# Performance work log

Measured on AMD Instinct MI355X. Metric: run time of the kernel, lower is better.

The kernel has to match this reference:

```python
import jax, jax.numpy as jnp
import numpy as np

V = 50257      # vocab size
H = 512        # hidden size
S = 128        # source length
BEAM = 5       # beam width (matches beam_width=5 default)
TMAX = 32      # MAX_LENGTH decode cap
SOS, EOS = 1, 2
NEG = -1e9


def setup_inputs() -> dict:
    key = jax.random.key(0)
    ks = jax.random.split(key, 12)
    p = lambda k, shape: jax.random.normal(k, shape, jnp.float32) * 0.02
    return {
        "input_tokens": jax.random.randint(ks[0], (S,), 0, V),
        "embedding": p(ks[1], (V, H)),
        "enc_Wih": p(ks[2], (3 * H, H)),
        "enc_Whh": p(ks[3], (3 * H, H)),
        "enc_bih": jnp.zeros((3 * H,), jnp.float32),
        "enc_bhh": jnp.zeros((3 * H,), jnp.float32),
        "dec_Wih": p(ks[4], (3 * H, H)),
        "dec_Whh": p(ks[5], (3 * H, H)),
        "dec_bih": jnp.zeros((3 * H,), jnp.float32),
        "dec_bhh": jnp.zeros((3 * H,), jnp.float32),
        "W_concat": p(ks[6], (2 * H, H)),
        "W_vocab": p(ks[7], (H, V)),
    }


def gru_cell(x, h, Wih, Whh, bih, bhh):
    # x, h: [..., H]
    gi = x @ Wih.T + bih
    gh = h @ Whh.T + bhh
    ir, iz, inn = jnp.split(gi, 3, -1)
    hr, hz, hn = jnp.split(gh, 3, -1)
    r = jax.nn.sigmoid(ir + hr)
    z = jax.nn.sigmoid(iz + hz)
    n = jnp.tanh(inn + r * hn)
    return (1.0 - z) * n + z * h


def reference(input_tokens, embedding, enc_Wih, enc_Whh, enc_bih, enc_bhh,
              dec_Wih, dec_Whh, dec_bih, dec_bhh, W_concat, W_vocab):
    # ---- encoder: 1-layer GRU over source tokens ----
    src_emb = embedding[input_tokens]                       # [S, H]

    def enc_step(h, x):
        h2 = gru_cell(x, h, enc_Wih, enc_Whh, enc_bih, enc_bhh)
        return h2, h2

    enc_h, enc_out = jax.lax.scan(enc_step, jnp.zeros((H,), src_emb.dtype), src_emb)
    # enc_out: [S, H], enc_h: [H]

    def decode_step(tokens, hidden):
        # tokens: [B] int, hidden: [B, H]
        x = embedding[tokens]                               # [B, H]
        h = gru_cell(x, hidden, dec_Wih, dec_Whh, dec_bih, dec_bhh)
        attn = jax.nn.softmax(h @ enc_out.T, axis=-1)       # [B, S] Luong dot attention
        ctx = attn @ enc_out                                # [B, H]
        o = jnp.tanh(jnp.concatenate([h, ctx], -1) @ W_concat)
        logp = jax.nn.log_softmax(o @ W_vocab, axis=-1)     # [B, V]
        return logp, h

    # ---- batched beam search (GPU-resident equivalent of the heapq loop) ----
    tokens0 = jnp.full((BEAM,), SOS, jnp.int32)
    hidden0 = jnp.tile(enc_h[None], (BEAM, 1))
    scores0 = jnp.full((BEAM,), NEG, jnp.float32).at[0].set(0.0)
    fin0 = jnp.zeros((BEAM,), bool)
    len0 = jnp.ones((BEAM,), jnp.int32)
    seqs0 = jnp.zeros((BEAM, TMAX), jnp.int32)
    fin_row = jnp.full((V,), NEG, jnp.float32).at[EOS].set(0.0)

    def beam_step(state, t):
        tokens, hidden, scores, finished, lengths, seqs = state
        logp, h2 = decode_step(tokens, hidden)              # [BEAM, V]
        step_lp = jnp.where(finished[:, None], fin_row[None, :], logp)
        cand = scores[:, None] + step_lp                    # [BEAM, V]
        top_scores, flat = jax.lax.top_k(cand.reshape(-1), BEAM)
        parent = flat // V
        tok = (flat % V).astype(jnp.int32)
        par_fin = finished[parent]
        new_fin = par_fin | (tok == EOS)
        new_len = lengths[parent] + jnp.where(par_fin, 0, 1)
        new_seqs = seqs[parent].at[:, t].set(jnp.where(par_fin, 0, tok))
        return (tok, h2[parent], top_scores, new_fin, new_len, new_seqs), None

    state, _ = jax.lax.scan(beam_step, (tokens0, hidden0, scores0, fin0, len0, seqs0),
                            jnp.arange(TMAX))
    _, _, scores, _, lengths, seqs = state
    # length-normalized ranking, matching node.logp / node.leng sort
    norm = scores / lengths.astype(scores.dtype)
    order = jnp.argsort(-norm)
    return seqs[order], norm[order]
```

## Files before the change

### kernel.cpp

```cpp
#include <hip/hip_runtime.h>
#include <cstdint>
#include <cstddef>

#define V_SZ 50257
#define H_SZ 512
#define S_SZ 128
#define NBEAM 5
#define TMAXX 32
#define TOK_SOS 1
#define TOK_EOS 2
#define NEGINF (-1e9f)

#define GW 128
#define NT 512
#define GENC 16
#define COLS_PER_WG 393

#define BI_LEAF(l)  ((l)*32)
#define BI_ROOT     256
#define BI_REL(l)   (512 + (l)*32)
#define BI_ECNT     1024
#define BI_EREL     1056

#define OF_GI    0
#define OF_ENC   196608
#define OF_EW    262144
#define OF_H2    327680
#define OF_AL    332800
#define OF_OTOP  333440
#define OF_PV    336000
#define OF_PM    339200
#define OF_PS    339840
#define OF_SC    340480
#define OI_BASE  340488

template <typename T>
__device__ __forceinline__ T aload(const T* p){
  return __hip_atomic_load((T*)p, __ATOMIC_RELAXED, __HIP_MEMORY_SCOPE_AGENT);
}
template <typename T>
__device__ __forceinline__ void astore(T* p, T v){
  __hip_atomic_store(p, v, __ATOMIC_RELAXED, __HIP_MEMORY_SCOPE_AGENT);
}

__device__ __forceinline__ float wredsum(float a){
#pragma unroll
  for (int m = 32; m; m >>= 1) a += __shfl_xor(a, m, 64);
  return a;
}

template <typename F>
__device__ __forceinline__ void dbar(int* bi, int wid, F&& tail){
  __shared__ int s_last;
  int mygen = 0;
  __syncthreads();
  if (threadIdx.x == 0){
    int leaf = wid >> 4;
    mygen = aload(bi + BI_REL(leaf));
    __builtin_amdgcn_s_waitcnt(0);
    int lo = __hip_atomic_fetch_add(bi + BI_LEAF(leaf), 1, __ATOMIC_RELAXED, __HIP_MEMORY_SCOPE_AGENT);
    int last = 0;
    if (lo == 15){
      astore(bi + BI_LEAF(leaf), 0);
      __builtin_amdgcn_s_waitcnt(0);
      int ro = __hip_atomic_fetch_add(bi + BI_ROOT, 1, __ATOMIC_RELAXED, __HIP_MEMORY_SCOPE_AGENT);
      if (ro == (GW/16) - 1){
        astore(bi + BI_ROOT, 0);
        last = 1;
      }
    }
    if (!last){
      while (aload(bi + BI_REL(leaf)) == mygen) __builtin_amdgcn_s_sleep(4);
    }
    s_last = last;
  }
  __syncthreads();
  if (s_last){
    tail();
    __syncthreads();
    if (threadIdx.x == 0){
      __builtin_amdgcn_s_waitcnt(0);
#pragma unroll
      for (int l = 0; l < GW/16; ++l) astore(bi + BI_REL(l), mygen + 1);
    }
  }
  __syncthreads();
}

__global__ __launch_bounds__(256)
void k_gi(const int* __restrict__ toks, const float* __restrict__ emb,
          const float* __restrict__ eWih, const float* __restrict__ ebih,
          float* __restrict__ ws)
{
  float* fb = ws + 2048;
  float* gi = fb + OF_GI;
  const int tid = threadIdx.x, wid = blockIdx.x, lane = tid & 63, wvi = tid >> 6;
  int Wg = wid*4 + wvi;
  for (int it = 0; it < 192; ++it){
    int idx = Wg*192 + it;
    int s = idx / 1536, j = idx - s*1536;
    const float* er = emb + (size_t)toks[s]*H_SZ;
    const float* wr = eWih + (size_t)j*H_SZ;
    float a = 0.f;
#pragma unroll
    for (int u = 0; u < 8; ++u) a += er[u*64+lane]*wr[u*64+lane];
    a = wredsum(a);
    if (lane == 0) gi[idx] = a + ebih[j];
  }
  if (wid == 0){
    float* sc = fb + OF_SC;
    int* ib = (int*)(fb + OI_BASE);
    if (tid < NBEAM){
      sc[tid] = (tid==0) ? 0.f : NEGINF;
      ib[3200+tid] = TOK_SOS; ib[3208+tid] = 0; ib[3216+tid] = 1; ib[3224+tid] = 0;
    }
    for (int q = tid; q < 2*NBEAM*TMAXX; q += 256) ib[3232+q] = 0;
  }
}

__global__ __launch_bounds__(NT, 1)
void k_enc(const float* __restrict__ eWhh, const float* __restrict__ ebhh,
           float* __restrict__ ws)
{
  int* bi = (int*)ws;
  float* fb = ws + 2048;
  float* gi = fb + OF_GI;
  float* enc = fb + OF_ENC;
  const int tid = threadIdx.x, wid = blockIdx.x, lane = tid & 63, wvi = tid >> 6;
  const int i0 = wid*32;
  __shared__ float smF[96];

  float wreg[12][8];
#pragma unroll
  for (int dd = 0; dd < 12; ++dd){
    int d = wvi*12 + dd, g = d >> 5, il = d & 31;
    const float* wr = eWhh + (size_t)(g*512 + i0 + il)*H_SZ;
#pragma unroll
    for (int u = 0; u < 8; ++u) wreg[dd][u] = wr[u*64+lane];
  }

  for (int s = 0; s < S_SZ; ++s){
    float hreg[8];
    if (s == 0){
#pragma unroll
      for (int u = 0; u < 8; ++u) hreg[u] = 0.f;
    } else {
      const float* hp = enc + (size_t)(s-1)*H_SZ;
#pragma unroll
      for (int u = 0; u < 8; ++u) hreg[u] = aload(hp + u*64 + lane);
    }
#pragma unroll
    for (int dd = 0; dd < 12; ++dd){
      float a = 0.f;
#pragma unroll
      for (int u = 0; u < 8; ++u) a += wreg[dd][u]*hreg[u];
      a = wredsum(a);
      if (lane == 0) smF[wvi*12 + dd] = a;
    }
    __syncthreads();
    if (tid < 32){
      int i = i0 + tid;
      float gr = smF[tid], gz = smF[32+tid], gn = smF[64+tid];
      float gir = gi[s*1536 + i], giz = gi[s*1536 + 512 + i], gin = gi[s*1536 + 1024 + i];
      float hprev = (s==0) ? 0.f : aload(enc + (s-1)*H_SZ + i);
      float r = 1.f/(1.f + expf(-(gir + gr + ebhh[i])));
      float z = 1.f/(1.f + expf(-(giz + gz + ebhh[512+i])));
      float n = tanhf(gin + r*(gn + ebhh[1024+i]));
      astore(enc + s*H_SZ + i, (1.f - z)*n + z*hprev);
    }
    __syncthreads();
    if (tid == 0){
      int g = aload(bi + BI_EREL);
      __builtin_amdgcn_s_waitcnt(0);
      int lo = __hip_atomic_fetch_add(bi + BI_ECNT, 1, __ATOMIC_RELAXED, __HIP_MEMORY_SCOPE_AGENT);
      if (lo == GENC - 1){
        astore(bi + BI_ECNT, 0);
        __builtin_amdgcn_s_waitcnt(0);
        astore(bi + BI_EREL, g + 1);
      } else {
        while (aload(bi + BI_EREL) == g) __builtin_amdgcn_s_sleep(2);
      }
    }
    __syncthreads();
  }
}

__global__ __launch_bounds__(NT)
void k_ew(const float* __restrict__ Wc, float* __restrict__ ws)
{
  float* fb = ws + 2048;
  float* enc = fb + OF_ENC;
  float* EW  = fb + OF_EW;
  const int tid = threadIdx.x, wid = blockIdx.x;
  int jc = wid & 15, sb = wid >> 4;
  int jl = tid & 31, sl = (tid >> 5) & 15;
  int s = sb*16 + sl, j = jc*32 + jl;
  const float* er = enc + (size_t)s*H_SZ;
  const float* wc = Wc + (size_t)512*H_SZ;
  float a = 0.f;
  for (int k = 0; k < 512; ++k) a += er[k]*wc[(size_t)k*H_SZ + j];
  EW[s*H_SZ + j] = a;
}

__global__ __launch_bounds__(NT, 1)
void k_dec(const float* __restrict__ emb,
           const float* __restrict__ dWih, const float* __restrict__ dWhh,
           const float* __restrict__ dbih, const float* __restrict__ dbhh,
           const float* __restrict__ Wc,  const float* __restrict__ Wv,
           float* __restrict__ out, float* __restrict__ ws)
{
  const int wid = blockIdx.x, tid = threadIdx.x;
  const int lane = tid & 63, wvi = tid >> 6;
  int* bi = (int*)ws;
  float* fb = ws + 2048;
  float* enc  = fb + OF_ENC;
  float* EW   = fb + OF_EW;
  float* h2   = fb + OF_H2;
  float* al   = fb + OF_AL;
  float* otop = fb + OF_OTOP;
  float* pv   = fb + OF_PV;
  float* pm   = fb + OF_PM;
  float* ps   = fb + OF_PS;
  float* sc   = fb + OF_SC;
  int* ib   = (int*)(fb + OI_BASE);
  int* pidx = ib;
  int* tokA = ib + 3200;
  int* finA = ib + 3208;
  int* lenA = ib + 3216;
  int* parA = ib + 3224;
  int* seqA = ib + 3232;

  __shared__ float smF[1024];
  __shared__ int   smI[256];
  __shared__ float s_buf[2560];
  __shared__ float s_pp[648];

  for (int t = 0; t < TMAXX; ++t){
    float* h2new = h2 + (t & 1)*2560;
    float* h2old = h2 + ((t & 1) ^ 1)*2560;

    if (tid < NBEAM){ smI[tid] = aload(tokA + tid); smI[8 + tid] = t ? aload(parA + tid) : 0; }
    __syncthreads();
    if (t == 0){
      for (int q = tid; q < 2560; q += NT) s_buf[q] = enc[127*H_SZ + (q & 511)];
    } else {
      for (int q = tid; q < 2560; q += NT){
        int b = q >> 9;
        s_buf[q] = aload(h2old + smI[8 + b]*H_SZ + (q & 511));
      }
    }
    __syncthreads();
    {
      int i0 = wid*4;
      int mat = wvi >> 2;
      float srg[5][8];
      if (mat == 0){
#pragma unroll
        for (int b = 0; b < NBEAM; ++b){
          const float* sp = emb + (size_t)smI[b]*H_SZ;
#pragma unroll
          for (int u = 0; u < 8; ++u) srg[b][u] = sp[u*64+lane];
        }
      } else {
#pragma unroll
        for (int b = 0; b < NBEAM; ++b)
#pragma unroll
          for (int u = 0; u < 8; ++u) srg[b][u] = s_buf[b*512 + u*64 + lane];
      }
      for (int rr = 0; rr < 3; ++rr){
        int R = wvi*3 + rr;
        int rem = R - mat*12;
        int g = rem >> 2, il = rem & 3;
        const float* wr = ((mat==0) ? dWih : dWhh) + (size_t)(g*512 + i0 + il)*H_SZ;
        float wreg[8];
#pragma unroll
        for (int u = 0; u < 8; ++u) wreg[u] = wr[u*64+lane];
#pragma unroll
        for (int b = 0; b < NBEAM; ++b){
          float a = 0.f;
#pragma unroll
          for (int u = 0; u < 8; ++u) a += wreg[u]*srg[b][u];
          a = wredsum(a);
          if (lane == 0) smF[R*5 + b] = a;
        }
      }
      __syncthreads();
      if (tid < 20){
        int b = tid >> 2, il = tid & 3;
        int i = i0 + il;
        float ir  = smF[(0*12 + 0*4 + il)*5 + b] + dbih[i];
        float iz  = smF[(0*12 + 1*4 + il)*5 + b] + dbih[512+i];
        float inn = smF[(0*12 + 2*4 + il)*5 + b] + dbih[1024+i];
        float hr  = smF[(1*12 + 0*4 + il)*5 + b] + dbhh[i];
        float hz  = smF[(1*12 + 1*4 + il)*5 + b] + dbhh[512+i];
        float hn  = smF[(1*12 + 2*4 + il)*5 + b] + dbhh[1024+i];
        float r = 1.f/(1.f + expf(-(ir + hr)));
        float z = 1.f/(1.f + expf(-(iz + hz)));
        float n = tanhf(inn + r*hn);
        float hp = s_buf[b*512 + i];
        astore(h2new + b*H_SZ + i, (1.f - z)*n + z*hp);
      }
    }
    dbar(bi, wid, [&](){});

    for (int q = tid; q < 2560; q += NT) s_buf[q] = aload(h2new + q);
    __syncthreads();
    if (wvi < NBEAM){
      const float* er = enc + (size_t)wid*H_SZ;
      float a = 0.f;
#pragma unroll
      for (int u = 0; u < 8; ++u) a += er[u*64+lane]*s_buf[wvi*512 + u*64 + lane];
      a = wredsum(a);
      if (lane == 0) astore(al + wvi*S_SZ + wid, a);
    }
    if (tid < 320){
      int q = tid % 20, ksl = tid / 20;
      int f = wid*20 + q;
      int b = f >> 9, j = f & 511;
      float a = 0.f;
#pragma unroll 8
      for (int u = 0; u < 32; ++u){
        int k = ksl*32 + u;
        a += s_buf[b*512 + k]*Wc[(size_t)k*H_SZ + j];
      }
      smF[q*16 + ksl] = a;
    }
    __syncthreads();
    if (tid < 20){
      float a = 0.f;
#pragma unroll
      for (int u = 0; u < 16; ++u) a += smF[tid*16 + u];
      astore(otop + wid*20 + tid, a);
    }
    dbar(bi, wid, [&](){});

    if (wvi < NBEAM){
      float a1 = aload(al + wvi*S_SZ + lane), a2 = aload(al + wvi*S_SZ + 64 + lane);
      float m = fmaxf(a1, a2);
#pragma unroll
      for (int mm = 32; mm; mm >>= 1) m = fmaxf(m, __shfl_xor(m, mm, 64));
      float e1 = expf(a1 - m), e2 = expf(a2 - m);
      s_pp[wvi*128 + lane] = e1; s_pp[wvi*128 + 64 + lane] = e2;
      float ssv = wredsum(e1 + e2);
      if (lane == 0) s_pp[640 + wvi] = ssv;
    }
    __syncthreads();
    {
      float acc[5] = {0.f,0.f,0.f,0.f,0.f};
      for (int s2 = 0; s2 < 128; ++s2){
        float e = EW[(size_t)s2*H_SZ + tid];
#pragma unroll
        for (int b = 0; b < NBEAM; ++b) acc[b] += e*s_pp[b*128 + s2];
      }
#pragma unroll
      for (int b = 0; b < NBEAM; ++b)
        s_buf[b*512 + tid] = tanhf(aload(otop + b*512 + tid) + acc[b]/s_pp[640 + b]);
    }
    __syncthreads();
    {
      int vbase = wid*COLS_PER_WG;
      int v = vbase + tid;
      bool act = (tid < COLS_PER_WG) && (v < V_SZ);
      int vc = act ? v : vbase;
      const float* wp = Wv + vc;
      float a0=0.f,a1=0.f,a2=0.f,a3=0.f,a4=0.f;
      for (int hb = 0; hb < H_SZ; hb += 16){
        float wr[16];
#pragma unroll
        for (int u = 0; u < 16; ++u) wr[u] = wp[(size_t)(hb+u)*V_SZ];
#pragma unroll
        for (int u = 0; u < 16; ++u){
          float w = wr[u];
          a0 += w*s_buf[hb+u];
          a1 += w*s_buf[512+hb+u];
          a2 += w*s_buf[1024+hb+u];
          a3 += w*s_buf[1536+hb+u];
          a4 += w*s_buf[2048+hb+u];
        }
      }
      if (!act){ a0=a1=a2=a3=a4=-3e38f; }
      int myv = act ? v : 0x7FFFFFFF;
      float accs[5] = {a0,a1,a2,a3,a4};
#pragma unroll
      for (int b = 0; b < NBEAM; ++b){
        float x = accs[b];
        float m = x;
#pragma unroll
        for (int mm = 32; mm; mm >>= 1) m = fmaxf(m, __shfl_xor(m, mm, 64));
        float e = expf(x - m);
        float ssum = wredsum(e);
        float bv = x; int bc = myv;
        float w5[5]; int i5[5];
#pragma unroll
        for (int r = 0; r < 5; ++r){
          float cv2 = bv; int ci2 = bc;
#pragma unroll
          for (int mm = 32; mm; mm >>= 1){
            float ov = __shfl_xor(cv2, mm, 64); int oi = __shfl_xor(ci2, mm, 64);
            bool take = (ov > cv2) || (ov == cv2 && oi < ci2);
            cv2 = take ? ov : cv2; ci2 = take ? oi : ci2;
          }
          w5[r] = cv2; i5[r] = ci2;
          if (bc == ci2) bv = -3e38f;
        }
        if (lane == 0){
#pragma unroll
          for (int r = 0; r < 5; ++r){ smF[(wvi*5+b)*5+r] = w5[r]; smI[(wvi*5+b)*5+r] = i5[r]; }
          smF[300 + wvi*5 + b] = m;
          smF[360 + wvi*5 + b] = ssum;
        }
      }
      __syncthreads();
      if (tid < NBEAM){
        float M = -3.4e38f, Sv = 0.f;
#pragma unroll
        for (int w8 = 0; w8 < 8; ++w8){
          float m2 = smF[300 + w8*5 + tid], s2 = smF[360 + w8*5 + tid];
          if (m2 > M){ Sv = Sv*expf(M - m2) + s2; M = m2; }
          else       { Sv = Sv + s2*expf(m2 - M); }
        }
        astore(pm + wid*5 + tid, M); astore(ps + wid*5 + tid, Sv);
      }
      if (wvi < NBEAM){
        int b = wvi;
        float cval; int cidx;
        if (lane < 40){ cval = smF[((lane/5)*5 + b)*5 + (lane%5)]; cidx = smI[((lane/5)*5 + b)*5 + (lane%5)]; }
        else { cval = -3e38f; cidx = 0x7FFFFFFF; }
        float bv = cval; int bc = cidx;
#pragma unroll
        for (int r = 0; r < 5; ++r){
          float cv2 = bv; int ci2 = bc;
#pragma unroll
          for (int mm = 32; mm; mm >>= 1){
            float ov = __shfl_xor(cv2, mm, 64); int oi = __shfl_xor(ci2, mm, 64);
            bool take = (ov > cv2) || (ov == cv2 && oi < ci2);
            cv2 = take ? ov : cv2; ci2 = take ? oi : ci2;
          }
          if (lane == 0){ astore(pv + (wid*5+b)*5+r, cv2); astore(pidx + (wid*5+b)*5+r, ci2); }
          if (bc == ci2) bv = -3e38f;
        }
      }
    }
    dbar(bi, wid, [&](){
      int b5 = wvi;
      if (b5 < NBEAM){
        float m1 = aload(pm + lane*5 + b5), s1 = aload(ps + lane*5 + b5);
        float m2 = aload(pm + (64+lane)*5 + b5), s2 = aload(ps + (64+lane)*5 + b5);
        float M, Sv;
        if (m1 >= m2){ M = m1; Sv = s1 + s2*expf(m2 - m1); }
        else         { M = m2; Sv = s2 + s1*expf(m1 - m2); }
#pragma unroll
        for (int mm = 32; mm; mm >>= 1){
          float om = __shfl_xor(M, mm, 64), os = __shfl_xor(Sv, mm, 64);
          if (om > M){ Sv = Sv*expf(M - om) + os; M = om; }
          else       { Sv = Sv + os*expf(om - M); }
        }
        if (lane == 0){ smF[8 + b5] = M; smF[80 + b5] = logf(Sv); }
        float lv[5]; int li[5];
#pragma unroll
        for (int r = 0; r < 5; ++r){ lv[r] = aload(pv + (lane*5 + b5)*5 + r); li[r] = aload(pidx + (lane*5 + b5)*5 + r); }
        for (int r = 0; r < 5; ++r){
          float nv = aload(pv + ((64+lane)*5 + b5)*5 + r); int ni = aload(pidx + ((64+lane)*5 + b5)*5 + r);
          bool ins = (nv > lv[4]) || (nv == lv[4] && ni < li[4]);
          if (!ins) break;
          lv[4] = nv; li[4] = ni;
#pragma unroll
          for (int p = 4; p > 0; --p){
            bool sw = (lv[p] > lv[p-1]) || (lv[p] == lv[p-1] && li[p] < li[p-1]);
            if (sw){ float tv = lv[p]; lv[p] = lv[p-1]; lv[p-1] = tv;
                     int ti = li[p]; li[p] = li[p-1]; li[p-1] = ti; }
          }
        }
        float cv = lv[0]; int ci = li[0];
#pragma unroll
        for (int r = 0; r < 5; ++r){
          float xv = cv; int xi = ci;
#pragma unroll
          for (int mm = 32; mm; mm >>= 1){
            float ov = __shfl_xor(xv, mm, 64); int oi = __shfl_xor(xi, mm, 64);
            bool take = (ov > xv) || (ov == xv && oi < xi);
            xv = take ? ov : xv; xi = take ? oi : xi;
          }
          if (lane == 0){ smF[16 + b5*5 + r] = xv; smI[16 + b5*5 + r] = xi; }
          if (ci == xi){
            lv[0]=lv[1]; li[0]=li[1]; lv[1]=lv[2]; li[1]=li[2];
            lv[2]=lv[3]; li[2]=li[3]; lv[3]=lv[4]; li[3]=li[4];
            lv[4] = -3e38f; li[4] = 0x7FFFFFFF;
            cv = lv[0]; ci = li[0];
          }
        }
      }
      __syncthreads();
      if (wvi == 0){
        float cval = -3e38f; int cflat = 0x7FFFFFFF;
        int b = lane/5, k = lane - b*5;
        if (lane < 25){
          if (aload(finA + b)){
            if (k == 0){ cval = aload(sc + b) + 0.0f; cflat = b*V_SZ + TOK_EOS; }
          } else {
            cval = ((smF[16 + b*5 + k] - smF[8 + b]) - smF[80 + b]) + aload(sc + b);
            cflat = b*V_SZ + smI[16 + b*5 + k];
          }
        }
        float bv = cval; int bc = cflat;
#pragma unroll
        for (int r = 0; r < 5; ++r){
          float xv = bv; int xi = bc;
#pragma unroll
          for (int mm = 32; mm; mm >>= 1){
            float ov = __shfl_xor(xv, mm, 64); int oi = __shfl_xor(xi, mm, 64);
            bool take = (ov > xv) || (ov == xv && oi < xi);
            xv = take ? ov : xv; xi = take ? oi : xi;
          }
          if (lane == 0){ smF[48 + r] = xv; smI[48 + r] = xi; }
          if (bc == xi) bv = -3e38f;
        }
        if (lane < NBEAM){
          int r = lane;
          float nscore = smF[48 + r]; int nfl = smI[48 + r];
          int par = nfl / V_SZ; int tok = nfl - par*V_SZ;
          int ofin = aload(finA + par); int olen = aload(lenA + par);
          int nf = (ofin || tok == TOK_EOS) ? 1 : 0;
          int nl = olen + (ofin ? 0 : 1);
          astore(sc + r, nscore); astore(tokA + r, tok); astore(finA + r, nf);
          astore(lenA + r, nl); astore(parA + r, par);
          smI[56 + r] = par; smI[64 + r] = tok; smI[72 + r] = ofin; smI[80 + r] = nl;
          smF[56 + r] = nscore;
        }
      }
      __syncthreads();
      int cur = t & 1, nxt = 1 - cur;
      if (tid < 160){
        int r = tid >> 5, u = tid & 31;
        int par = smI[56 + r];
        int val = aload(seqA + cur*160 + par*32 + u);
        if (u == t) val = smI[72 + r] ? 0 : smI[64 + r];
        astore(seqA + nxt*160 + r*32 + u, val);
      }
      if (t == TMAXX - 1){
        __syncthreads();
        if (tid == 0){
          float nn[5];
#pragma unroll
          for (int r = 0; r < 5; ++r) nn[r] = smF[56 + r] / (float)smI[80 + r];
          int used = 0;
#pragma unroll
          for (int r = 0; r < 5; ++r){
            int best = -1;
            for (int q2 = 0; q2 < 5; ++q2){
              if (used & (1 << q2)) continue;
              if (best < 0 || nn[q2] > nn[best]) best = q2;
            }
            used |= (1 << best);
            smI[88 + r] = best; smF[64 + r] = nn[best];
          }
        }
        __syncthreads();
        if (tid < 160){
          int r = tid >> 5, u = tid & 31;
          int src = smI[88 + r];
          out[tid] = (float)aload(seqA + nxt*160 + src*32 + u);
        }
        if (tid >= 160 && tid < 165) out[tid] = smF[64 + (tid - 160)];
      }
    });
  }
}

extern "C" void kernel_launch(void* const* d_in, const int* in_sizes, int n_in,
                              void* d_out, int out_size, void* d_ws, size_t ws_size,
                              hipStream_t stream)
{
  (void)in_sizes; (void)n_in; (void)out_size; (void)ws_size;
  hipMemsetAsync(d_ws, 0, 8192, stream);
  float* ws = (float*)d_ws;
  k_gi<<<dim3(256), dim3(256), 0, stream>>>(
      (const int*)d_in[0], (const float*)d_in[1],
      (const float*)d_in[2], (const float*)d_in[4], ws);
  k_enc<<<dim3(GENC), dim3(NT), 0, stream>>>(
      (const float*)d_in[3], (const float*)d_in[5], ws);
  k_ew<<<dim3(128), dim3(NT), 0, stream>>>(
      (const float*)d_in[10], ws);
  k_dec<<<dim3(GW), dim3(NT), 0, stream>>>(
      (const float*)d_in[1],
      (const float*)d_in[6], (const float*)d_in[7],
      (const float*)d_in[8], (const float*)d_in[9],
      (const float*)d_in[10], (const float*)d_in[11],
      (float*)d_out, ws);
}
```

Baseline: 3.696 ms.

## Double decoder workgroups, split vocab GEMV by K-halves, use per-step flag encoder sync

```diff
diff --git a/kernel.cpp b/kernel.cpp
--- a/kernel.cpp
+++ b/kernel.cpp
@@ -11,16 +11,17 @@
 #define TOK_EOS 2
 #define NEGINF (-1e9f)
 
-#define GW 128
+#define GW 256
 #define NT 512
 #define GENC 16
-#define COLS_PER_WG 393
+#define COLS_PER_WG 200
 
 #define BI_LEAF(l)  ((l)*32)
-#define BI_ROOT     256
-#define BI_REL(l)   (512 + (l)*32)
-#define BI_ECNT     1024
-#define BI_EREL     1056
+#define BI_ROOT     544
+#define BI_REL(l)   (576 + (l)*32)
+#define BI_EFLAG    1152
+
+#define FB_OFF 4096
 
 #define OF_GI    0
 #define OF_ENC   196608
@@ -29,10 +30,10 @@
 #define OF_AL    332800
 #define OF_OTOP  333440
 #define OF_PV    336000
-#define OF_PM    339200
-#define OF_PS    339840
-#define OF_SC    340480
-#define OI_BASE  340488
+#define OF_PM    342400
+#define OF_PS    343680
+#define OF_SC    344960
+#define OI_BASE  344968
 
 template <typename T>
 __device__ __forceinline__ T aload(const T* p){
@@ -92,7 +93,7 @@
           const float* __restrict__ eWih, const float* __restrict__ ebih,
           float* __restrict__ ws)
 {
-  float* fb = ws + 2048;
+  float* fb = ws + FB_OFF;
   float* gi = fb + OF_GI;
   const int tid = threadIdx.x, wid = blockIdx.x, lane = tid & 63, wvi = tid >> 6;
   int Wg = wid*4 + wvi;
@@ -112,9 +113,9 @@
     int* ib = (int*)(fb + OI_BASE);
     if (tid < NBEAM){
       sc[tid] = (tid==0) ? 0.f : NEGINF;
-      ib[3200+tid] = TOK_SOS; ib[3208+tid] = 0; ib[3216+tid] = 1; ib[3224+tid] = 0;
-    }
-    for (int q = tid; q < 2*NBEAM*TMAXX; q += 256) ib[3232+q] = 0;
+      ib[6400+tid] = TOK_SOS; ib[6408+tid] = 0; ib[6416+tid] = 1; ib[6424+tid] = 0;
+    }
+    for (int q = tid; q < 2*NBEAM*TMAXX; q += 256) ib[6432+q] = 0;
   }
 }
 
@@ -123,7 +124,7 @@
            float* __restrict__ ws)
 {
   int* bi = (int*)ws;
-  float* fb = ws + 2048;
+  float* fb = ws + FB_OFF;
   float* gi = fb + OF_GI;
   float* enc = fb + OF_ENC;
   const int tid = threadIdx.x, wid = blockIdx.x, lane = tid & 63, wvi = tid >> 6;
@@ -145,6 +146,10 @@
 #pragma unroll
       for (int u = 0; u < 8; ++u) hreg[u] = 0.f;
     } else {
+      if (tid < 16){
+        while (aload(bi + BI_EFLAG + (s-1)*16 + tid) == 0) __builtin_amdgcn_s_sleep(1);
+      }
+      __syncthreads();
       const float* hp = enc + (size_t)(s-1)*H_SZ;
 #pragma unroll
       for (int u = 0; u < 8; ++u) hreg[u] = aload(hp + u*64 + lane);
@@ -170,25 +175,16 @@
     }
     __syncthreads();
     if (tid == 0){
-      int g = aload(bi + BI_EREL);
       __builtin_amdgcn_s_waitcnt(0);
-      int lo = __hip_atomic_fetch_add(bi + BI_ECNT, 1, __ATOMIC_RELAXED, __HIP_MEMORY_SCOPE_AGENT);
-      if (lo == GENC - 1){
-        astore(bi + BI_ECNT, 0);
-        __builtin_amdgcn_s_waitcnt(0);
-        astore(bi + BI_EREL, g + 1);
-      } else {
-        while (aload(bi + BI_EREL) == g) __builtin_amdgcn_s_sleep(2);
-      }
-    }
-    __syncthreads();
+      astore(bi + BI_EFLAG + s*16 + wid, 1);
+    }
   }
 }
 
 __global__ __launch_bounds__(NT)
 void k_ew(const float* __restrict__ Wc, float* __restrict__ ws)
 {
-  float* fb = ws + 2048;
+  float* fb = ws + FB_OFF;
   float* enc = fb + OF_ENC;
   float* EW  = fb + OF_EW;
   const int tid = threadIdx.x, wid = blockIdx.x;
@@ -202,7 +198,7 @@
   EW[s*H_SZ + j] = a;
 }
 
-__global__ __launch_bounds__(NT, 1)
+__global__ __launch_bounds__(NT, 4)
 void k_dec(const float* __restrict__ emb,
            const float* __restrict__ dWih, const float* __restrict__ dWhh,
            const float* __restrict__ dbih, const float* __restrict__ dbhh,
@@ -212,7 +208,7 @@
   const int wid = blockIdx.x, tid = threadIdx.x;
   const int lane = tid & 63, wvi = tid >> 6;
   int* bi = (int*)ws;
-  float* fb = ws + 2048;
+  float* fb = ws + FB_OFF;
   float* enc  = fb + OF_ENC;
   float* EW   = fb + OF_EW;
   float* h2   = fb + OF_H2;
@@ -224,13 +220,13 @@
   float* sc   = fb + OF_SC;
   int* ib   = (int*)(fb + OI_BASE);
   int* pidx = ib;
-  int* tokA = ib + 3200;
-  int* finA = ib + 3208;
-  int* lenA = ib + 3216;
-  int* parA = ib + 3224;
-  int* seqA = ib + 3232;
-
-  __shared__ float smF[1024];
+  int* tokA = ib + 6400;
+  int* finA = ib + 6408;
+  int* lenA = ib + 6416;
+  int* parA = ib + 6424;
+  int* seqA = ib + 6432;
+
+  __shared__ float smF[2048];
   __shared__ int   smI[256];
   __shared__ float s_buf[2560];
   __shared__ float s_pp[648];
@@ -239,18 +235,18 @@
     float* h2new = h2 + (t & 1)*2560;
     float* h2old = h2 + ((t & 1) ^ 1)*2560;
 
-    if (tid < NBEAM){ smI[tid] = aload(tokA + tid); smI[8 + tid] = t ? aload(parA + tid) : 0; }
-    __syncthreads();
-    if (t == 0){
-      for (int q = tid; q < 2560; q += NT) s_buf[q] = enc[127*H_SZ + (q & 511)];
-    } else {
-      for (int q = tid; q < 2560; q += NT){
-        int b = q >> 9;
-        s_buf[q] = aload(h2old + smI[8 + b]*H_SZ + (q & 511));
-      }
-    }
-    __syncthreads();
-    {
+    if (wid < 128){
+      if (tid < NBEAM){ smI[tid] = aload(tokA + tid); smI[8 + tid] = t ? aload(parA + tid) : 0; }
+      __syncthreads();
+      if (t == 0){
+        for (int q = tid; q < 2560; q += NT) s_buf[q] = enc[127*H_SZ + (q & 511)];
+      } else {
+        for (int q = tid; q < 2560; q += NT){
+          int b = q >> 9;
+          s_buf[q] = aload(h2old + smI[8 + b]*H_SZ + (q & 511));
+        }
+      }
+      __syncthreads();
       int i0 = wid*4;
       int mat = wvi >> 2;
       float srg[5][8];
@@ -305,7 +301,7 @@
 
     for (int q = tid; q < 2560; q += NT) s_buf[q] = aload(h2new + q);
     __syncthreads();
-    if (wvi < NBEAM){
+    if (wid < 128 && wvi < NBEAM){
       const float* er = enc + (size_t)wid*H_SZ;
       float a = 0.f;
 #pragma unroll
@@ -313,9 +309,9 @@
       a = wredsum(a);
       if (lane == 0) astore(al + wvi*S_SZ + wid, a);
     }
-    if (tid < 320){
-      int q = tid % 20, ksl = tid / 20;
-      int f = wid*20 + q;
+    if (tid < 160){
+      int q = tid % 10, ksl = tid / 10;
+      int f = wid*10 + q;
       int b = f >> 9, j = f & 511;
       float a = 0.f;
 #pragma unroll 8
@@ -326,11 +322,11 @@
       smF[q*16 + ksl] = a;
     }
     __syncthreads();
-    if (tid < 20){
+    if (tid < 10){
       float a = 0.f;
 #pragma unroll
       for (int u = 0; u < 16; ++u) a += smF[tid*16 + u];
-      astore(otop + wid*20 + tid, a);
+      astore(otop + wid*10 + tid, a);
     }
     dbar(bi, wid, [&](){});
 
@@ -352,70 +348,90 @@
 #pragma unroll
         for (int b = 0; b < NBEAM; ++b) acc[b] += e*s_pp[b*128 + s2];
       }
+      float ov[5];
 #pragma unroll
       for (int b = 0; b < NBEAM; ++b)
-        s_buf[b*512 + tid] = tanhf(aload(otop + b*512 + tid) + acc[b]/s_pp[640 + b]);
+        ov[b] = tanhf(aload(otop + b*512 + tid) + acc[b]/s_pp[640 + b]);
+      __syncthreads();
+#pragma unroll
+      for (int b = 0; b < NBEAM; ++b) s_buf[b*512 + tid] = ov[b];
     }
     __syncthreads();
     {
-      int vbase = wid*COLS_PER_WG;
-      int v = vbase + tid;
-      bool act = (tid < COLS_PER_WG) && (v < V_SZ);
-      int vc = act ? v : vbase;
+      const int c = tid & 255;
+      const int half = tid >> 8;
+      const int vbase = wid*COLS_PER_WG;
+      const int v = vbase + c;
+      const bool act = (c < COLS_PER_WG) && (v < V_SZ);
+      const int vc = act ? v : (V_SZ - 1);
       const float* wp = Wv + vc;
-      float a0=0.f,a1=0.f,a2=0.f,a3=0.f,a4=0.f;
-      for (int hb = 0; hb < H_SZ; hb += 16){
+      const int r0 = half*256;
+      float acc[5] = {0.f,0.f,0.f,0.f,0.f};
+      for (int hb = r0; hb < r0 + 256; hb += 16){
         float wr[16];
 #pragma unroll
-        for (int u = 0; u < 16; ++u) wr[u] = wp[(size_t)(hb+u)*V_SZ];
+        for (int u = 0; u < 16; ++u) wr[u] = __builtin_nontemporal_load(wp + (size_t)(hb+u)*V_SZ);
 #pragma unroll
         for (int u = 0; u < 16; ++u){
           float w = wr[u];
-          a0 += w*s_buf[hb+u];
-          a1 += w*s_buf[512+hb+u];
-          a2 += w*s_buf[1024+hb+u];
-          a3 += w*s_buf[1536+hb+u];
-          a4 += w*s_buf[2048+hb+u];
-        }
-      }
-      if (!act){ a0=a1=a2=a3=a4=-3e38f; }
-      int myv = act ? v : 0x7FFFFFFF;
-      float accs[5] = {a0,a1,a2,a3,a4};
-#pragma unroll
-      for (int b = 0; b < NBEAM; ++b){
-        float x = accs[b];
-        float m = x;
-#pragma unroll
-        for (int mm = 32; mm; mm >>= 1) m = fmaxf(m, __shfl_xor(m, mm, 64));
-        float e = expf(x - m);
-        float ssum = wredsum(e);
-        float bv = x; int bc = myv;
-        float w5[5]; int i5[5];
-#pragma unroll
-        for (int r = 0; r < 5; ++r){
-          float cv2 = bv; int ci2 = bc;
-#pragma unroll
-          for (int mm = 32; mm; mm >>= 1){
-            float ov = __shfl_xor(cv2, mm, 64); int oi = __shfl_xor(ci2, mm, 64);
-            bool take = (ov > cv2) || (ov == cv2 && oi < ci2);
-            cv2 = take ? ov : cv2; ci2 = take ? oi : ci2;
-          }
-          w5[r] = cv2; i5[r] = ci2;
-          if (bc == ci2) bv = -3e38f;
-        }
-        if (lane == 0){
-#pragma unroll
-          for (int r = 0; r < 5; ++r){ smF[(wvi*5+b)*5+r] = w5[r]; smI[(wvi*5+b)*5+r] = i5[r]; }
-          smF[300 + wvi*5 + b] = m;
-          smF[360 + wvi*5 + b] = ssum;
+          acc[0] += w*s_buf[hb+u];
+          acc[1] += w*s_buf[512+hb+u];
+          acc[2] += w*s_buf[1024+hb+u];
+          acc[3] += w*s_buf[1536+hb+u];
+          acc[4] += w*s_buf[2048+hb+u];
+        }
+      }
+      if (c < COLS_PER_WG){
+#pragma unroll
+        for (int b = 0; b < NBEAM; ++b) smF[(half*COLS_PER_WG + c)*5 + b] = acc[b];
+      }
+      __syncthreads();
+      float x5[5]; int myv = 0x7FFFFFFF;
+      bool act2 = (tid < COLS_PER_WG) && (vbase + tid < V_SZ);
+      if (tid < 256){
+#pragma unroll
+        for (int b = 0; b < NBEAM; ++b)
+          x5[b] = act2 ? (smF[tid*5 + b] + smF[(COLS_PER_WG + tid)*5 + b]) : -3e38f;
+        if (act2) myv = vbase + tid;
+      }
+      __syncthreads();
+      if (wvi < 4){
+#pragma unroll
+        for (int b = 0; b < NBEAM; ++b){
+          float x = x5[b];
+          float m = x;
+#pragma unroll
+          for (int mm = 32; mm; mm >>= 1) m = fmaxf(m, __shfl_xor(m, mm, 64));
+          float e = expf(x - m);
+          float ssum = wredsum(e);
+          float bv = x; int bc = myv;
+          float w5[5]; int i5[5];
+#pragma unroll
+          for (int r = 0; r < 5; ++r){
+            float cv2 = bv; int ci2 = bc;
+#pragma unroll
+            for (int mm = 32; mm; mm >>= 1){
+              float ovl = __shfl_xor(cv2, mm, 64); int oi = __shfl_xor(ci2, mm, 64);
+              bool take = (ovl > cv2) || (ovl == cv2 && oi < ci2);
+              cv2 = take ? ovl : cv2; ci2 = take ? oi : ci2;
+            }
+            w5[r] = cv2; i5[r] = ci2;
+            if (bc == ci2) bv = -3e38f;
+          }
+          if (lane == 0){
+#pragma unroll
+            for (int r = 0; r < 5; ++r){ smF[(wvi*5+b)*5+r] = w5[r]; smI[(wvi*5+b)*5+r] = i5[r]; }
+            smF[600 + wvi*5 + b] = m;
+            smF[700 + wvi*5 + b] = ssum;
+          }
         }
       }
       __syncthreads();
       if (tid < NBEAM){
         float M = -3.4e38f, Sv = 0.f;
 #pragma unroll
-        for (int w8 = 0; w8 < 8; ++w8){
-          float m2 = smF[300 + w8*5 + tid], s2 = smF[360 + w8*5 + tid];
+        for (int w4 = 0; w4 < 4; ++w4){
+          float m2 = smF[600 + w4*5 + tid], s2 = smF[700 + w4*5 + tid];
           if (m2 > M){ Sv = Sv*expf(M - m2) + s2; M = m2; }
           else       { Sv = Sv + s2*expf(m2 - M); }
         }
@@ -424,7 +440,7 @@
       if (wvi < NBEAM){
         int b = wvi;
         float cval; int cidx;
-        if (lane < 40){ cval = smF[((lane/5)*5 + b)*5 + (lane%5)]; cidx = smI[((lane/5)*5 + b)*5 + (lane%5)]; }
+        if (lane < 20){ cval = smF[((lane/5)*5 + b)*5 + (lane%5)]; cidx = smI[((lane/5)*5 + b)*5 + (lane%5)]; }
         else { cval = -3e38f; cidx = 0x7FFFFFFF; }
         float bv = cval; int bc = cidx;
 #pragma unroll
@@ -432,9 +448,9 @@
           float cv2 = bv; int ci2 = bc;
 #pragma unroll
           for (int mm = 32; mm; mm >>= 1){
-            float ov = __shfl_xor(cv2, mm, 64); int oi = __shfl_xor(ci2, mm, 64);
-            bool take = (ov > cv2) || (ov == cv2 && oi < ci2);
-            cv2 = take ? ov : cv2; ci2 = take ? oi : ci2;
+            float ovl = __shfl_xor(cv2, mm, 64); int oi = __shfl_xor(ci2, mm, 64);
+            bool take = (ovl > cv2) || (ovl == cv2 && oi < ci2);
+            cv2 = take ? ovl : cv2; ci2 = take ? oi : ci2;
           }
           if (lane == 0){ astore(pv + (wid*5+b)*5+r, cv2); astore(pidx + (wid*5+b)*5+r, ci2); }
           if (bc == ci2) bv = -3e38f;
@@ -444,11 +460,13 @@
     dbar(bi, wid, [&](){
       int b5 = wvi;
       if (b5 < NBEAM){
-        float m1 = aload(pm + lane*5 + b5), s1 = aload(ps + lane*5 + b5);
-        float m2 = aload(pm + (64+lane)*5 + b5), s2 = aload(ps + (64+lane)*5 + b5);
-        float M, Sv;
-        if (m1 >= m2){ M = m1; Sv = s1 + s2*expf(m2 - m1); }
-        else         { M = m2; Sv = s2 + s1*expf(m1 - m2); }
+        float M = aload(pm + lane*5 + b5), Sv = aload(ps + lane*5 + b5);
+#pragma unroll
+        for (int g = 1; g < 4; ++g){
+          float m2 = aload(pm + (g*64+lane)*5 + b5), s2 = aload(ps + (g*64+lane)*5 + b5);
+          if (m2 > M){ Sv = Sv*expf(M - m2) + s2; M = m2; }
+          else       { Sv = Sv + s2*expf(m2 - M); }
+        }
 #pragma unroll
         for (int mm = 32; mm; mm >>= 1){
           float om = __shfl_xor(M, mm, 64), os = __shfl_xor(Sv, mm, 64);
@@ -459,16 +477,19 @@
         float lv[5]; int li[5];
 #pragma unroll
         for (int r = 0; r < 5; ++r){ lv[r] = aload(pv + (lane*5 + b5)*5 + r); li[r] = aload(pidx + (lane*5 + b5)*5 + r); }
-        for (int r = 0; r < 5; ++r){
-          float nv = aload(pv + ((64+lane)*5 + b5)*5 + r); int ni = aload(pidx + ((64+lane)*5 + b5)*5 + r);
-          bool ins = (nv > lv[4]) || (nv == lv[4] && ni < li[4]);
-          if (!ins) break;
-          lv[4] = nv; li[4] = ni;
-#pragma unroll
-          for (int p = 4; p > 0; --p){
-            bool sw = (lv[p] > lv[p-1]) || (lv[p] == lv[p-1] && li[p] < li[p-1]);
-            if (sw){ float tv = lv[p]; lv[p] = lv[p-1]; lv[p-1] = tv;
-                     int ti = li[p]; li[p] = li[p-1]; li[p-1] = ti; }
+#pragma unroll
+        for (int g = 1; g < 4; ++g){
+          for (int r = 0; r < 5; ++r){
+            float nv = aload(pv + ((g*64+lane)*5 + b5)*5 + r); int ni = aload(pidx + ((g*64+lane)*5 + b5)*5 + r);
+            bool ins = (nv > lv[4]) || (nv == lv[4] && ni < li[4]);
+            if (!ins) break;
+            lv[4] = nv; li[4] = ni;
+#pragma unroll
+            for (int p = 4; p > 0; --p){
+              bool sw = (lv[p] > lv[p-1]) || (lv[p] == lv[p-1] && li[p] < li[p-1]);
+              if (sw){ float tv = lv[p]; lv[p] = lv[p-1]; lv[p-1] = tv;
+                       int ti = li[p]; li[p] = li[p-1]; li[p-1] = ti; }
+            }
           }
         }
         float cv = lv[0]; int ci = li[0];
@@ -477,9 +498,9 @@
           float xv = cv; int xi = ci;
 #pragma unroll
           for (int mm = 32; mm; mm >>= 1){
-            float ov = __shfl_xor(xv, mm, 64); int oi = __shfl_xor(xi, mm, 64);
-            bool take = (ov > xv) || (ov == xv && oi < xi);
-            xv = take ? ov : xv; xi = take ? oi : xi;
+            float ovl = __shfl_xor(xv, mm, 64); int oi = __shfl_xor(xi, mm, 64);
+            bool take = (ovl > xv) || (ovl == xv && oi < xi);
+            xv = take ? ovl : xv; xi = take ? oi : xi;
           }
           if (lane == 0){ smF[16 + b5*5 + r] = xv; smI[16 + b5*5 + r] = xi; }
           if (ci == xi){
@@ -508,9 +529,9 @@
           float xv = bv; int xi = bc;
 #pragma unroll
           for (int mm = 32; mm; mm >>= 1){
-            float ov = __shfl_xor(xv, mm, 64); int oi = __shfl_xor(xi, mm, 64);
-            bool take = (ov > xv) || (ov == xv && oi < xi);
-            xv = take ? ov : xv; xi = take ? oi : xi;
+            float ovl = __shfl_xor(xv, mm, 64); int oi = __shfl_xor(xi, mm, 64);
+            bool take = (ovl > xv) || (ovl == xv && oi < xi);
+            xv = take ? ovl : xv; xi = take ? oi : xi;
           }
           if (lane == 0){ smF[48 + r] = xv; smI[48 + r] = xi; }
           if (bc == xi) bv = -3e38f;
@@ -572,7 +593,7 @@
                               hipStream_t stream)
 {
   (void)in_sizes; (void)n_in; (void)out_size; (void)ws_size;
-  hipMemsetAsync(d_ws, 0, 8192, stream);
+  hipMemsetAsync(d_ws, 0, 16384, stream);
   float* ws = (float*)d_ws;
   k_gi<<<dim3(256), dim3(256), 0, stream>>>(
       (const int*)d_in[0], (const float*)d_in[1],
```

New measurement: 4.599 ms. 24.4% more time.
